# Optimization experiments

Measured on AMD Instinct MI355X. Metric: run time of the kernel, lower is better.

Reference implementation:

```python
import jax, jax.numpy as jnp
import numpy as np

B, F = 8192, 256
H1, H2, H3 = 32, 64, 32
ORDER = 2
OUT = 1


def setup_inputs() -> dict:
    key = jax.random.key(0)
    ks = jax.random.split(key, 6)
    x = jax.random.normal(ks[0], (B, F), dtype=jnp.float32)
    # stacked per-feature FeatureNet weights, fan-in scaled to keep ReLUs active
    W1 = jax.random.normal(ks[1], (F, 1, H1), dtype=jnp.float32) * 1.0
    b1 = jnp.zeros((F, H1), dtype=jnp.float32)
    W2 = jax.random.normal(ks[2], (F, H1, H2), dtype=jnp.float32) * (1.0 / np.sqrt(H1))
    b2 = jnp.zeros((F, H2), dtype=jnp.float32)
    W3 = jax.random.normal(ks[3], (F, H2, H3), dtype=jnp.float32) * (1.0 / np.sqrt(H2))
    b3 = jnp.zeros((F, H3), dtype=jnp.float32)
    Wout = jax.random.normal(ks[4], (ORDER * H3, OUT), dtype=jnp.float32) * (1.0 / np.sqrt(ORDER * H3))
    bout = jnp.zeros((OUT,), dtype=jnp.float32)
    return {"x": x, "W1": W1, "b1": b1, "W2": W2, "b2": b2,
            "W3": W3, "b3": b3, "Wout": Wout, "bout": bout}


def _feature_nets(x, W1, b1, W2, b2, W3, b3):
    # x: [B, F] -> per-feature tiny MLP 1->32->64->32, batched over F
    h = jax.nn.relu(x[:, :, None] * W1[:, 0, :][None] + b1[None])      # [B, F, 32]
    h = jax.nn.relu(jnp.einsum('bfh,fho->bfo', h, W2) + b2[None])       # [B, F, 64]
    h = jax.nn.relu(jnp.einsum('bfh,fho->bfo', h, W3) + b3[None])       # [B, F, 32]
    return h


def reference(x, W1, b1, W2, b2, W3, b3, Wout, bout):
    t = _feature_nets(x, W1, b1, W2, b2, W3, b3)  # [B, F, H3]
    # Newton's identity power-sum recurrence over interaction order
    p1 = t.sum(axis=1)                            # [B, H3]
    powers = [None, p1]                           # powers[0] unused (scalar 1 in orig)
    inters = [jnp.ones_like(p1), p1]              # interactions[0] = 1 (broadcast)
    for i in range(2, ORDER + 1):
        powers.append(jnp.power(t, i).sum(axis=1))
        cur = 0.0
        for j in range(1, i + 1):
            cur = cur + ((-1.0) ** (j + 1)) * powers[j] * inters[i - j]
        inters.append(cur / i)
    feats = jnp.concatenate(inters[1:], axis=1)   # [B, ORDER*H3]
    pred = feats @ Wout + bout                    # [B, OUT]
    return pred
```

## Files before the change

kernel.cpp:

```cpp
#include <hip/hip_runtime.h>
#include <hip/hip_bf16.h>

#define B_   8192
#define F_   256
#define NFC  16
#define NF   (F_/NFC)
#define RPB  128
#define NSUB 2

typedef __attribute__((ext_vector_type(8))) short v8s;
typedef __attribute__((ext_vector_type(4))) float v4f;
typedef __attribute__((ext_vector_type(4))) unsigned int v4u;

static __device__ __forceinline__ unsigned short f2bf(float f) {
    __hip_bfloat16 h = __float2bfloat16(f);
    return __builtin_bit_cast(unsigned short, h);
}

static __device__ __forceinline__ unsigned cvtpk(float a, float b) {
    unsigned r;
    asm("v_cvt_pk_bf16_f32 %0, %1, %2" : "=v"(r) : "v"(a), "v"(b));
    return r;
}

static __device__ __forceinline__ void gload_lds16(const void* g, void* l) {
    __builtin_amdgcn_global_load_lds(
        (const __attribute__((address_space(1))) unsigned int*)g,
        (__attribute__((address_space(3))) unsigned int*)l,
        16, 0, 0);
}

__global__ __launch_bounds__(256)
void honam_prep(const float* __restrict__ w2g, const float* __restrict__ w3g,
                const float* __restrict__ w1g, const float* __restrict__ b1g,
                const float* __restrict__ b2g, const float* __restrict__ b3g,
                unsigned short* __restrict__ wf, float* __restrict__ pp)
{
    const int f   = blockIdx.x;
    const int tid = threadIdx.x;
    const float* w2 = w2g + (size_t)f * 2048;
    const float* w3 = w3g + (size_t)f * 2048;
    unsigned short* dst = wf + (size_t)f * 4096;
    for (int i = tid; i < 4096; i += 256) {
        const int frag = i >> 9;
        const int l    = (i >> 3) & 63;
        const int j    = i & 7;
        const int c    = l & 15;
        const int g    = l >> 4;
        float v;
        if (frag < 4) {
            v = w2[(g * 8 + j) * 64 + frag * 16 + c];
        } else {
            const int kk = (frag - 4) >> 1;
            const int n2 = (frag - 4) & 1;
            const int u  = (kk * 2 + (j >> 2)) * 16 + g * 4 + (j & 3);
            v = w3[u * 32 + n2 * 16 + c];
        }
        dst[i] = f2bf(v);
    }
    if (tid < 160) {
        float v;
        if (tid < 32)       v = w1g[f * 32 + tid];
        else if (tid < 64)  v = b1g[f * 32 + (tid - 32)];
        else if (tid < 128) v = b2g[f * 64 + (tid - 64)];
        else                v = b3g[f * 32 + (tid - 128)];
        pp[(size_t)f * 160 + tid] = v;
    }
}

__global__ __launch_bounds__(256, 4)
void honam_k1(const float* __restrict__ xg,
              const unsigned short* __restrict__ wfg, const float* __restrict__ ppg,
              float* __restrict__ p1part, float* __restrict__ p2part)
{
    __shared__ float xs[NF][RPB];
    __shared__ float ps[NF * 160];
    __shared__ short wbuf[2][4096] __attribute__((aligned(16)));

    const int tid  = threadIdx.x;
    const int wave = tid >> 6;
    const int lane = tid & 63;
    const int c16  = lane & 15;
    const int g4   = lane >> 4;

    const int bx = blockIdx.x;
    const int rb = bx >> 4;
    const int fc = bx & 15;
    const int r0 = rb * RPB;
    const int f0 = fc * NF;

    {
        const int row  = tid >> 1;
        const int half = tid & 1;
        const float4 va = *(const float4*)&xg[(size_t)(r0 + row) * F_ + f0 + half * 8];
        const float4 vb = *(const float4*)&xg[(size_t)(r0 + row) * F_ + f0 + half * 8 + 4];
        const int fb = half * 8;
        xs[fb + 0][row] = va.x; xs[fb + 1][row] = va.y;
        xs[fb + 2][row] = va.z; xs[fb + 3][row] = va.w;
        xs[fb + 4][row] = vb.x; xs[fb + 5][row] = vb.y;
        xs[fb + 6][row] = vb.z; xs[fb + 7][row] = vb.w;
    }
    {
        const float4* src = (const float4*)(ppg + (size_t)f0 * 160);
        float4* dst = (float4*)ps;
        dst[tid]       = src[tid];
        dst[tid + 256] = src[tid + 256];
        if (tid < 128) dst[tid + 512] = src[tid + 512];
    }
    {
        const char* src = (const char*)wfg + (size_t)f0 * 8192 + (2 * wave) * 1024 + lane * 16;
        gload_lds16(src,        &wbuf[0][(2 * wave) * 512]);
        gload_lds16(src + 1024, &wbuf[0][(2 * wave + 1) * 512]);
    }
    __syncthreads();

    float pacc1[NSUB][2][4];
    float pacc2[NSUB][2][4];
#pragma unroll
    for (int s = 0; s < NSUB; ++s)
#pragma unroll
        for (int n2 = 0; n2 < 2; ++n2)
#pragma unroll
            for (int j = 0; j < 4; ++j) { pacc1[s][n2][j] = 0.f; pacc2[s][n2][j] = 0.f; }

#pragma unroll 2
    for (int fi = 0; fi < NF; ++fi) {
        const int cur = fi & 1;
        if (fi + 1 < NF) {
            const char* src = (const char*)wfg + (size_t)(f0 + fi + 1) * 8192
                            + (2 * wave) * 1024 + lane * 16;
            gload_lds16(src,        &wbuf[cur ^ 1][(2 * wave) * 512]);
            gload_lds16(src + 1024, &wbuf[cur ^ 1][(2 * wave + 1) * 512]);
        }
        v8s wfr[8];
#pragma unroll
        for (int fr = 0; fr < 8; ++fr)
            wfr[fr] = *(const v8s*)&wbuf[cur][fr * 512 + lane * 8];

        const float4 w1a = *(const float4*)&ps[fi * 160 + g4 * 8];
        const float4 w1b = *(const float4*)&ps[fi * 160 + g4 * 8 + 4];
        const float4 b1a = *(const float4*)&ps[fi * 160 + 32 + g4 * 8];
        const float4 b1b = *(const float4*)&ps[fi * 160 + 32 + g4 * 8 + 4];
        const float w1v[8] = {w1a.x, w1a.y, w1a.z, w1a.w, w1b.x, w1b.y, w1b.z, w1b.w};
        const float b1v[8] = {b1a.x, b1a.y, b1a.z, b1a.w, b1b.x, b1b.y, b1b.z, b1b.w};
        float4 b2c[4];
#pragma unroll
        for (int n = 0; n < 4; ++n)
            b2c[n] = *(const float4*)&ps[fi * 160 + 64 + n * 16 + g4 * 4];
        float b3v[2];
#pragma unroll
        for (int n = 0; n < 2; ++n) b3v[n] = ps[fi * 160 + 128 + n * 16 + c16];

        float xm[NSUB];
#pragma unroll
        for (int s = 0; s < NSUB; ++s)
            xm[s] = xs[fi][s * 64 + wave * 16 + c16];

#pragma unroll
        for (int sub = 0; sub < NSUB; ++sub) {
            unsigned h1p[4];
#pragma unroll
            for (int jj = 0; jj < 4; ++jj) {
                const float e0 = fmaxf(fmaf(xm[sub], w1v[2 * jj],     b1v[2 * jj]),     0.f);
                const float e1 = fmaxf(fmaf(xm[sub], w1v[2 * jj + 1], b1v[2 * jj + 1]), 0.f);
                h1p[jj] = cvtpk(e0, e1);
            }
            const v8s bh1 = __builtin_bit_cast(v8s, (v4u){h1p[0], h1p[1], h1p[2], h1p[3]});

            v4f acc2[4];
#pragma unroll
            for (int n = 0; n < 4; ++n)
                acc2[n] = __builtin_amdgcn_mfma_f32_16x16x32_bf16(
                    wfr[n], bh1, (v4f){b2c[n].x, b2c[n].y, b2c[n].z, b2c[n].w}, 0, 0, 0);

            unsigned q[8];
#pragma unroll
            for (int n = 0; n < 4; ++n) {
                q[2 * n]     = cvtpk(fmaxf(acc2[n][0], 0.f), fmaxf(acc2[n][1], 0.f));
                q[2 * n + 1] = cvtpk(fmaxf(acc2[n][2], 0.f), fmaxf(acc2[n][3], 0.f));
            }
            const v8s a2k0 = __builtin_bit_cast(v8s, (v4u){q[0], q[1], q[2], q[3]});
            const v8s a2k1 = __builtin_bit_cast(v8s, (v4u){q[4], q[5], q[6], q[7]});

            v4f acc3[2];
#pragma unroll
            for (int n2 = 0; n2 < 2; ++n2) {
                acc3[n2] = __builtin_amdgcn_mfma_f32_16x16x32_bf16(
                    a2k0, wfr[4 + n2], (v4f){b3v[n2], b3v[n2], b3v[n2], b3v[n2]}, 0, 0, 0);
                acc3[n2] = __builtin_amdgcn_mfma_f32_16x16x32_bf16(
                    a2k1, wfr[6 + n2], acc3[n2], 0, 0, 0);
            }
#pragma unroll
            for (int n2 = 0; n2 < 2; ++n2)
#pragma unroll
                for (int j = 0; j < 4; ++j) {
                    const float t = fmaxf(acc3[n2][j], 0.f);
                    pacc1[sub][n2][j] += t;
                    pacc2[sub][n2][j] = fmaf(t, t, pacc2[sub][n2][j]);
                }
        }
        __syncthreads();
    }

    float* p1c = p1part + (size_t)fc * (B_ * 32);
    float* p2c = p2part + (size_t)fc * (B_ * 32);
#pragma unroll
    for (int sub = 0; sub < NSUB; ++sub)
#pragma unroll
        for (int n2 = 0; n2 < 2; ++n2)
#pragma unroll
            for (int j = 0; j < 4; ++j) {
                const int row = r0 + sub * 64 + wave * 16 + g4 * 4 + j;
                const int col = n2 * 16 + c16;
                p1c[row * 32 + col] = pacc1[sub][n2][j];
                p2c[row * 32 + col] = pacc2[sub][n2][j];
            }
}

__global__ __launch_bounds__(256)
void honam_k2(const float* __restrict__ p1part, const float* __restrict__ p2part,
              const float* __restrict__ woutg, const float* __restrict__ boutg,
              float* __restrict__ outg)
{
    const int tid = threadIdx.x;
    const int o   = tid & 31;
    const int r   = blockIdx.x * 8 + (tid >> 5);
    const size_t idx = (size_t)r * 32 + o;

    float s1 = 0.f, s2 = 0.f;
#pragma unroll
    for (int fc = 0; fc < NFC; ++fc) {
        s1 += p1part[(size_t)fc * (B_ * 32) + idx];
        s2 += p2part[(size_t)fc * (B_ * 32) + idx];
    }
    const float wa = woutg[o];
    const float wb = woutg[32 + o];
    float val = s1 * wa + 0.5f * (s1 * s1 - s2) * wb;
#pragma unroll
    for (int off = 16; off > 0; off >>= 1)
        val += __shfl_down(val, off, 32);
    if (o == 0) outg[r] = val + boutg[0];
}

extern "C" void kernel_launch(void* const* d_in, const int* in_sizes, int n_in,
                              void* d_out, int out_size, void* d_ws, size_t ws_size,
                              hipStream_t stream)
{
    const float* xg    = (const float*)d_in[0];
    const float* w1g   = (const float*)d_in[1];
    const float* b1g   = (const float*)d_in[2];
    const float* w2g   = (const float*)d_in[3];
    const float* b2g   = (const float*)d_in[4];
    const float* w3g   = (const float*)d_in[5];
    const float* b3g   = (const float*)d_in[6];
    const float* woutg = (const float*)d_in[7];
    const float* boutg = (const float*)d_in[8];
    float* outg = (float*)d_out;

    float* p1part = (float*)d_ws;
    float* p2part = p1part + (size_t)NFC * B_ * 32;
    unsigned short* wf = (unsigned short*)(p2part + (size_t)NFC * B_ * 32);
    float* pp = (float*)(wf + (size_t)F_ * 4096);

    honam_prep<<<dim3(F_), dim3(256), 0, stream>>>(w2g, w3g, w1g, b1g, b2g, b3g, wf, pp);

    honam_k1<<<dim3((B_ / RPB) * NFC), dim3(256), 0, stream>>>(
        xg, wf, pp, p1part, p2part);

    honam_k2<<<dim3(B_ / 8), dim3(256), 0, stream>>>(p1part, p2part, woutg, boutg, outg);
}
```

Before: 52.99 us.

## Stage two features per phase and halve barriers in feature MLP kernel

The weight double-buffer is restructured so each pipeline phase stages and computes two features instead of one. This halves the number of __syncthreads barriers and gives the async global-to-LDS loads more compute to hide behind. LDS use doubles for the weight buffers, so the launch bound drops from 4 to 3 blocks per CU, which may reduce occupancy. Accumulators are also repacked as float2 pairs, and the b2 bias loads move inside the MFMA loop.

```diff
diff --git a/kernel.cpp b/kernel.cpp
--- a/kernel.cpp
+++ b/kernel.cpp
@@ -5,6 +5,7 @@
 #define F_   256
 #define NFC  16
 #define NF   (F_/NFC)
+#define NPH  (NF/2)
 #define RPB  128
 #define NSUB 2
 
@@ -68,14 +69,14 @@
     }
 }
 
-__global__ __launch_bounds__(256, 4)
+__global__ __launch_bounds__(256, 3)
 void honam_k1(const float* __restrict__ xg,
               const unsigned short* __restrict__ wfg, const float* __restrict__ ppg,
               float* __restrict__ p1part, float* __restrict__ p2part)
 {
     __shared__ float xs[NF][RPB];
     __shared__ float ps[NF * 160];
-    __shared__ short wbuf[2][4096] __attribute__((aligned(16)));
+    __shared__ short wbuf[2][2][4096] __attribute__((aligned(16)));
 
     const int tid  = threadIdx.x;
     const int wave = tid >> 6;
@@ -107,54 +108,52 @@
         dst[tid + 256] = src[tid + 256];
         if (tid < 128) dst[tid + 512] = src[tid + 512];
     }
-    {
-        const char* src = (const char*)wfg + (size_t)f0 * 8192 + (2 * wave) * 1024 + lane * 16;
-        gload_lds16(src,        &wbuf[0][(2 * wave) * 512]);
-        gload_lds16(src + 1024, &wbuf[0][(2 * wave + 1) * 512]);
-    }
+
+    auto stage = [&](int set, int fp, int fl) {
+        const char* src = (const char*)wfg + (size_t)(f0 + fl) * 8192
+                        + (2 * wave) * 1024 + lane * 16;
+        gload_lds16(src,        &wbuf[set][fp][(2 * wave) * 512]);
+        gload_lds16(src + 1024, &wbuf[set][fp][(2 * wave + 1) * 512]);
+    };
+
+    stage(0, 0, 0);
+    stage(0, 1, 1);
     __syncthreads();
 
-    float pacc1[NSUB][2][4];
-    float pacc2[NSUB][2][4];
+    float2 pacc1[NSUB][2][2];
+    float2 pacc2[NSUB][2][2];
 #pragma unroll
     for (int s = 0; s < NSUB; ++s)
 #pragma unroll
         for (int n2 = 0; n2 < 2; ++n2)
 #pragma unroll
-            for (int j = 0; j < 4; ++j) { pacc1[s][n2][j] = 0.f; pacc2[s][n2][j] = 0.f; }
-
-#pragma unroll 2
-    for (int fi = 0; fi < NF; ++fi) {
-        const int cur = fi & 1;
-        if (fi + 1 < NF) {
-            const char* src = (const char*)wfg + (size_t)(f0 + fi + 1) * 8192
-                            + (2 * wave) * 1024 + lane * 16;
-            gload_lds16(src,        &wbuf[cur ^ 1][(2 * wave) * 512]);
-            gload_lds16(src + 1024, &wbuf[cur ^ 1][(2 * wave + 1) * 512]);
-        }
+            for (int jp = 0; jp < 2; ++jp) {
+                pacc1[s][n2][jp] = make_float2(0.f, 0.f);
+                pacc2[s][n2][jp] = make_float2(0.f, 0.f);
+            }
+
+    auto computeFeat = [&](int set, int fp, int fl) {
+        const short* wb = &wbuf[set][fp][0];
         v8s wfr[8];
 #pragma unroll
         for (int fr = 0; fr < 8; ++fr)
-            wfr[fr] = *(const v8s*)&wbuf[cur][fr * 512 + lane * 8];
-
-        const float4 w1a = *(const float4*)&ps[fi * 160 + g4 * 8];
-        const float4 w1b = *(const float4*)&ps[fi * 160 + g4 * 8 + 4];
-        const float4 b1a = *(const float4*)&ps[fi * 160 + 32 + g4 * 8];
-        const float4 b1b = *(const float4*)&ps[fi * 160 + 32 + g4 * 8 + 4];
+            wfr[fr] = *(const v8s*)&wb[fr * 512 + lane * 8];
+
+        const int fb = fl * 160;
+        const float4 w1a = *(const float4*)&ps[fb + g4 * 8];
+        const float4 w1b = *(const float4*)&ps[fb + g4 * 8 + 4];
+        const float4 b1a = *(const float4*)&ps[fb + 32 + g4 * 8];
+        const float4 b1b = *(const float4*)&ps[fb + 32 + g4 * 8 + 4];
         const float w1v[8] = {w1a.x, w1a.y, w1a.z, w1a.w, w1b.x, w1b.y, w1b.z, w1b.w};
         const float b1v[8] = {b1a.x, b1a.y, b1a.z, b1a.w, b1b.x, b1b.y, b1b.z, b1b.w};
-        float4 b2c[4];
-#pragma unroll
-        for (int n = 0; n < 4; ++n)
-            b2c[n] = *(const float4*)&ps[fi * 160 + 64 + n * 16 + g4 * 4];
         float b3v[2];
 #pragma unroll
-        for (int n = 0; n < 2; ++n) b3v[n] = ps[fi * 160 + 128 + n * 16 + c16];
+        for (int n = 0; n < 2; ++n) b3v[n] = ps[fb + 128 + n * 16 + c16];
 
         float xm[NSUB];
 #pragma unroll
         for (int s = 0; s < NSUB; ++s)
-            xm[s] = xs[fi][s * 64 + wave * 16 + c16];
+            xm[s] = xs[fl][s * 64 + wave * 16 + c16];
 
 #pragma unroll
         for (int sub = 0; sub < NSUB; ++sub) {
@@ -169,9 +168,10 @@
 
             v4f acc2[4];
 #pragma unroll
-            for (int n = 0; n < 4; ++n)
-                acc2[n] = __builtin_amdgcn_mfma_f32_16x16x32_bf16(
-                    wfr[n], bh1, (v4f){b2c[n].x, b2c[n].y, b2c[n].z, b2c[n].w}, 0, 0, 0);
+            for (int n = 0; n < 4; ++n) {
+                const v4f b2cv = *(const v4f*)&ps[fb + 64 + n * 16 + g4 * 4];
+                acc2[n] = __builtin_amdgcn_mfma_f32_16x16x32_bf16(wfr[n], bh1, b2cv, 0, 0, 0);
+            }
 
             unsigned q[8];
 #pragma unroll
@@ -193,12 +193,27 @@
 #pragma unroll
             for (int n2 = 0; n2 < 2; ++n2)
 #pragma unroll
-                for (int j = 0; j < 4; ++j) {
-                    const float t = fmaxf(acc3[n2][j], 0.f);
-                    pacc1[sub][n2][j] += t;
-                    pacc2[sub][n2][j] = fmaf(t, t, pacc2[sub][n2][j]);
+                for (int jp = 0; jp < 2; ++jp) {
+                    float2 t;
+                    t.x = fmaxf(acc3[n2][2 * jp],     0.f);
+                    t.y = fmaxf(acc3[n2][2 * jp + 1], 0.f);
+                    pacc1[sub][n2][jp].x += t.x;
+                    pacc1[sub][n2][jp].y += t.y;
+                    pacc2[sub][n2][jp].x += t.x * t.x;
+                    pacc2[sub][n2][jp].y += t.y * t.y;
                 }
         }
+    };
+
+#pragma unroll 2
+    for (int ph = 0; ph < NPH; ++ph) {
+        const int set = ph & 1;
+        if (ph + 1 < NPH) {
+            stage(set ^ 1, 0, 2 * ph + 2);
+            stage(set ^ 1, 1, 2 * ph + 3);
+        }
+        computeFeat(set, 0, 2 * ph);
+        computeFeat(set, 1, 2 * ph + 1);
         __syncthreads();
     }
 
@@ -209,11 +224,13 @@
 #pragma unroll
         for (int n2 = 0; n2 < 2; ++n2)
 #pragma unroll
-            for (int j = 0; j < 4; ++j) {
-                const int row = r0 + sub * 64 + wave * 16 + g4 * 4 + j;
+            for (int jp = 0; jp < 2; ++jp) {
+                const int row = r0 + sub * 64 + wave * 16 + g4 * 4 + 2 * jp;
                 const int col = n2 * 16 + c16;
-                p1c[row * 32 + col] = pacc1[sub][n2][j];
-                p2c[row * 32 + col] = pacc2[sub][n2][j];
+                p1c[row * 32 + col]       = pacc1[sub][n2][jp].x;
+                p1c[(row + 1) * 32 + col] = pacc1[sub][n2][jp].y;
+                p2c[row * 32 + col]       = pacc2[sub][n2][jp].x;
+                p2c[(row + 1) * 32 + col] = pacc2[sub][n2][jp].y;
             }
 }
 
```

Result: faster. 50.13 us (-5.4%).
